# Optimization experiments

Hardware: AMD Instinct MI355X
Metric: run time of the kernel (lower is better)

Reference implementation:

```python
import jax, jax.numpy as jnp
import numpy as np
import math

E = 1024
H = 16
R = 16
ALPHA = 16
SCALING = ALPHA / R
T, B, S = 2048, 2, 2048


def setup_inputs() -> dict:
    key = jax.random.key(0)
    ks = jax.random.split(key, 20)
    d = {
        "query": jax.random.normal(ks[0], (T, B, E), jnp.float32),
        "key": jax.random.normal(ks[1], (S, B, E), jnp.float32),
        "value": jax.random.normal(ks[2], (S, B, E), jnp.float32),
    }
    i = 3
    for name in ("q", "k", "v", "o"):
        d[name + "_w"] = jax.random.normal(ks[i], (E, E), jnp.float32) * 0.02; i += 1
        d[name + "_b"] = jax.random.normal(ks[i], (E,), jnp.float32) * 0.02; i += 1
        d[name + "_la"] = jax.random.normal(ks[i], (R, E), jnp.float32) * 0.02; i += 1
        d[name + "_lb"] = jax.random.normal(ks[i], (E, R), jnp.float32) * 0.02; i += 1
    return d


def _lora_linear(x, w, b, la, lb):
    # y = x @ w.T + b + scaling * (x @ la.T) @ lb.T
    return x @ w.T + b + SCALING * ((x @ la.T) @ lb.T)


def reference(query, key, value,
              q_w, q_b, q_la, q_lb,
              k_w, k_b, k_la, k_lb,
              v_w, v_b, v_la, v_lb,
              o_w, o_b, o_la, o_lb):
    tgt_len, bsz, embed_dim = query.shape
    src_len = key.shape[0]
    head_dim = embed_dim // H
    q = _lora_linear(query, q_w, q_b, q_la, q_lb)
    k = _lora_linear(key, k_w, k_b, k_la, k_lb)
    v = _lora_linear(value, v_w, v_b, v_la, v_lb)
    # (T, B, E) -> (B*H, T, hd)
    q = q.reshape(tgt_len, bsz * H, head_dim).transpose(1, 0, 2)
    k = k.reshape(src_len, bsz * H, head_dim).transpose(1, 0, 2)
    v = v.reshape(src_len, bsz * H, head_dim).transpose(1, 0, 2)
    scale = 1.0 / math.sqrt(float(head_dim))
    scores = jnp.einsum("btd,bsd->bts", q * scale, k)  # (B*H, T, S)
    attn = jax.nn.softmax(scores, axis=-1)
    out = jnp.einsum("bts,bsd->btd", attn, v)  # (B*H, T, hd)
    out = out.transpose(1, 0, 2).reshape(tgt_len * bsz, embed_dim)
    out = _lora_linear(out, o_w, o_b, o_la, o_lb)
    out = out.reshape(tgt_len, bsz, embed_dim)
    attn_w = attn.reshape(bsz, H, tgt_len, src_len).mean(axis=1)
    return out, attn_w
```

## Files before the change

### kernel.cpp

```cpp
#include <hip/hip_runtime.h>
#include <stdint.h>

#define E_DIM 1024
#define KAUG 1056
#define N_HEADS 16
#define HD 64
#define R_LORA 16
#define T_LEN 2048
#define B_SZ 2
#define S_LEN 2048
#define NROW 4096
#define Q_SCALE 0.1803368801111204f

#define XG_N ((size_t)NROW * KAUG)
#define WG_N ((size_t)E_DIM * KAUG)
#define HSZ  ((size_t)B_SZ * N_HEADS * T_LEN * HD)

typedef unsigned short USH;
typedef __bf16 bf16x8 __attribute__((ext_vector_type(8)));
typedef unsigned short ushort8 __attribute__((ext_vector_type(8)));
typedef float  f32x4  __attribute__((ext_vector_type(4)));
typedef float  f32x16 __attribute__((ext_vector_type(16)));
typedef unsigned int u32x2 __attribute__((ext_vector_type(2)));
typedef unsigned int u32x4 __attribute__((ext_vector_type(4)));

__device__ __forceinline__ USH f2bf(float f) {
    uint32_t u = __builtin_bit_cast(uint32_t, f);
    return (USH)((u + 0x7FFFu + ((u >> 16) & 1u)) >> 16);
}
__device__ __forceinline__ float bf2f(USH s) {
    uint32_t u = ((uint32_t)s) << 16;
    return __builtin_bit_cast(float, u);
}
__device__ __forceinline__ void async_cp16(const void* g, void* l) {
    __builtin_amdgcn_global_load_lds(
        (const __attribute__((address_space(1))) void*)g,
        (__attribute__((address_space(3))) void*)l, 16, 0, 0);
}
__device__ __forceinline__ uint32_t pack_bf_trunc(float x, float y) {
    return __builtin_amdgcn_perm(__builtin_bit_cast(uint32_t, y),
                                 __builtin_bit_cast(uint32_t, x), 0x07060302u);
}
__device__ __forceinline__ bf16x8 cvt8(float4 a, float4 b) {
    ushort8 u;
    u[0] = f2bf(a.x); u[1] = f2bf(a.y); u[2] = f2bf(a.z); u[3] = f2bf(a.w);
    u[4] = f2bf(b.x); u[5] = f2bf(b.y); u[6] = f2bf(b.z); u[7] = f2bf(b.w);
    return __builtin_bit_cast(bf16x8, u);
}

__global__ __launch_bounds__(256) void lora_aug_x3_kernel(
    const float* __restrict__ Xq, const float* __restrict__ Xk,
    const float* __restrict__ Xv,
    const float* __restrict__ laq, const float* __restrict__ lak,
    const float* __restrict__ lav, USH* __restrict__ Xg_base) {
    int n0 = blockIdx.x * 16, y = blockIdx.y, tid = threadIdx.x;
    const float* X  = (y == 0) ? Xq : (y == 1) ? Xk : Xv;
    const float* la = (y == 0) ? laq : (y == 1) ? lak : lav;
    USH* Xg = Xg_base + (size_t)y * XG_N;

    int w = tid >> 6, lane = tid & 63, quad = lane >> 4, l16 = lane & 15;

    const float* xrow = X + (size_t)(n0 + l16) * E_DIM;
    const float* lrow = la + (size_t)l16 * E_DIM;
    USH* grow = Xg + (size_t)(n0 + l16) * KAUG;

    const f32x4 fzero = {0.f, 0.f, 0.f, 0.f};
    f32x4 acc = fzero;

#pragma unroll
    for (int i = 0; i < 8; ++i) {
        int k = w * 256 + i * 32 + quad * 8;
        bf16x8 af = cvt8(*(const float4*)(xrow + k), *(const float4*)(xrow + k + 4));
        *(bf16x8*)(grow + k) = af;
        bf16x8 bf_ = cvt8(*(const float4*)(lrow + k), *(const float4*)(lrow + k + 4));
        acc = __builtin_amdgcn_mfma_f32_16x16x32_bf16(af, bf_, acc, 0, 0, 0);
    }

    __shared__ float red[4][16][17];
#pragma unroll
    for (int r = 0; r < 4; ++r) red[w][quad * 4 + r][l16] = acc[r];
    __syncthreads();

    int row = tid >> 4, col = tid & 15;
    float v = red[0][row][col] + red[1][row][col] + red[2][row][col] + red[3][row][col];
    USH* trow = Xg + (size_t)(n0 + row) * KAUG + 1024;
    trow[col] = f2bf(v);
    trow[16 + col] = (col == 0) ? f2bf(1.0f) : (USH)0;
}

__global__ __launch_bounds__(256) void lora_a_bf16_kernel(
    USH* __restrict__ Xg, const float* __restrict__ la) {
    int n0 = blockIdx.x * 16, tid = threadIdx.x;
    int w = tid >> 6, lane = tid & 63, quad = lane >> 4, l16 = lane & 15;

    const USH* grow = Xg + (size_t)(n0 + l16) * KAUG;
    const float* lrow = la + (size_t)l16 * E_DIM;

    const f32x4 fzero = {0.f, 0.f, 0.f, 0.f};
    f32x4 acc = fzero;

#pragma unroll
    for (int i = 0; i < 8; ++i) {
        int k = w * 256 + i * 32 + quad * 8;
        bf16x8 af = *(const bf16x8*)(grow + k);
        bf16x8 bf_ = cvt8(*(const float4*)(lrow + k), *(const float4*)(lrow + k + 4));
        acc = __builtin_amdgcn_mfma_f32_16x16x32_bf16(af, bf_, acc, 0, 0, 0);
    }

    __shared__ float red[4][16][17];
#pragma unroll
    for (int r = 0; r < 4; ++r) red[w][quad * 4 + r][l16] = acc[r];
    __syncthreads();

    int row = tid >> 4, col = tid & 15;
    float v = red[0][row][col] + red[1][row][col] + red[2][row][col] + red[3][row][col];
    USH* trow = Xg + (size_t)(n0 + row) * KAUG + 1024;
    trow[col] = f2bf(v);
    trow[16 + col] = (col == 0) ? f2bf(1.0f) : (USH)0;
}

__global__ __launch_bounds__(256) void aug_w4_kernel(
    const float* __restrict__ Wq, const float* __restrict__ lbq, const float* __restrict__ bq,
    const float* __restrict__ Wk, const float* __restrict__ lbk, const float* __restrict__ bk_,
    const float* __restrict__ Wv, const float* __restrict__ lbv, const float* __restrict__ bv_,
    const float* __restrict__ Wo, const float* __restrict__ lbo, const float* __restrict__ bo,
    USH* __restrict__ Wg_base) {
    int e = blockIdx.x, y = blockIdx.y, tid = threadIdx.x;
    const float* W    = (y == 0) ? Wq : (y == 1) ? Wk : (y == 2) ? Wv : Wo;
    const float* lb   = (y == 0) ? lbq : (y == 1) ? lbk : (y == 2) ? lbv : lbo;
    const float* bias = (y == 0) ? bq : (y == 1) ? bk_ : (y == 2) ? bv_ : bo;
    USH* Wg = Wg_base + (size_t)y * WG_N;

    float4 v = *(const float4*)(W + (size_t)e * E_DIM + tid * 4);
    ushort4 o;
    o.x = f2bf(v.x); o.y = f2bf(v.y); o.z = f2bf(v.z); o.w = f2bf(v.w);
    *(ushort4*)(Wg + (size_t)e * KAUG + tid * 4) = o;
    if (tid < 32) {
        float t = (tid < R_LORA) ? lb[(size_t)e * R_LORA + tid]
                                 : (tid == R_LORA ? bias[e] : 0.0f);
        Wg[(size_t)e * KAUG + 1024 + tid] = f2bf(t);
    }
}

__global__ __launch_bounds__(256) void gemm_qkv_kernel(
    const USH* __restrict__ Xg_base, const USH* __restrict__ Wg_base,
    USH* __restrict__ qkv_base) {
    __shared__ __align__(16) USH As[2][128 * 32];
    __shared__ __align__(16) USH Bs[2][128 * 32];

    int orig = blockIdx.x + (blockIdx.y << 3) + blockIdx.z * 256;
    int v_ = (orig & 7) * 96 + (orig >> 3);
    int e0 = (v_ & 7) * 128, n0 = ((v_ >> 3) & 31) * 128, z = v_ >> 8;

    const USH* Xg = Xg_base + (size_t)z * XG_N;
    const USH* Wg = Wg_base + (size_t)z * WG_N;
    USH* out = qkv_base + (size_t)z * HSZ;
    float scale = (z == 0) ? Q_SCALE : 1.0f;

    int tid = threadIdx.x;
    int wid = tid >> 6, lane = tid & 63, quad = lane >> 4, l16 = lane & 15;
    int wm = wid & 1, wn = wid >> 1;

    int r0 = wid * 16 + (lane >> 2);
    int k8 = (lane & 3) * 8;

    f32x4 acc[4][4];
    const f32x4 fzero = {0.f, 0.f, 0.f, 0.f};
#pragma unroll
    for (int i = 0; i < 4; ++i)
#pragma unroll
        for (int j = 0; j < 4; ++j) acc[i][j] = fzero;

    async_cp16(Xg + (size_t)(n0 + r0) * KAUG + k8,       As[0] + (wid * 16) * 32);
    async_cp16(Xg + (size_t)(n0 + 64 + r0) * KAUG + k8,  As[0] + (64 + wid * 16) * 32);
    async_cp16(Wg + (size_t)(e0 + r0) * KAUG + k8,       Bs[0] + (wid * 16) * 32);
    async_cp16(Wg + (size_t)(e0 + 64 + r0) * KAUG + k8,  Bs[0] + (64 + wid * 16) * 32);
    __syncthreads();

    int cur = 0;
    for (int kt = 0; kt < KAUG; kt += 32, cur ^= 1) {
        if (kt + 32 < KAUG) {
            int kn = kt + 32;
            async_cp16(Xg + (size_t)(n0 + r0) * KAUG + kn + k8,       As[cur ^ 1] + (wid * 16) * 32);
            async_cp16(Xg + (size_t)(n0 + 64 + r0) * KAUG + kn + k8,  As[cur ^ 1] + (64 + wid * 16) * 32);
            async_cp16(Wg + (size_t)(e0 + r0) * KAUG + kn + k8,       Bs[cur ^ 1] + (wid * 16) * 32);
            async_cp16(Wg + (size_t)(e0 + 64 + r0) * KAUG + kn + k8,  Bs[cur ^ 1] + (64 + wid * 16) * 32);
        }

        bf16x8 af[4], bfr[4];
#pragma unroll
        for (int i = 0; i < 4; ++i)
            af[i] = *(const bf16x8*)&As[cur][(wm * 64 + i * 16 + l16) * 32 + quad * 8];
#pragma unroll
        for (int j = 0; j < 4; ++j)
            bfr[j] = *(const bf16x8*)&Bs[cur][(wn * 64 + j * 16 + l16) * 32 + quad * 8];
#pragma unroll
        for (int i = 0; i < 4; ++i)
#pragma unroll
            for (int j = 0; j < 4; ++j)
                acc[i][j] = __builtin_amdgcn_mfma_f32_16x16x32_bf16(
                    af[i], bfr[j], acc[i][j], 0, 0, 0);

        __syncthreads();
    }

#pragma unroll
    for (int i = 0; i < 4; ++i) {
#pragma unroll
        for (int j = 0; j < 4; ++j) {
#pragma unroll
            for (int r = 0; r < 4; ++r) {
                int nr = n0 + wm * 64 + i * 16 + quad * 4 + r;
                int ec = e0 + wn * 64 + j * 16 + l16;
                float v = acc[i][j][r] * scale;
                int b = nr & 1, h = ec >> 6, d = ec & 63;
                if (z != 2) {
                    int t = nr >> 1;
                    out[(((size_t)(b * 16 + h) * T_LEN + t) << 6) + d] = f2bf(v);
                } else {
                    int s = nr >> 1;
                    out[(((size_t)(b * 16 + h) * HD + d) << 11) + s] = f2bf(v);
                }
            }
        }
    }
}

__global__ __launch_bounds__(256) void gemm_o_kernel(
    const USH* __restrict__ Xg, const USH* __restrict__ Wg,
    float* __restrict__ out) {
    __shared__ __align__(16) USH As[2][64 * 32];
    __shared__ __align__(16) USH Bs[2][128 * 32];

    int orig = blockIdx.x + (blockIdx.y << 3);
    int v_ = ((orig & 7) << 6) + (orig >> 3);
    int e0 = (v_ & 7) * 128, n0 = (v_ >> 3) * 64;

    int tid = threadIdx.x;
    int wid = tid >> 6, lane = tid & 63, quad = lane >> 4, l16 = lane & 15;
    int wm = wid & 1, wn = wid >> 1;
    int r0 = wid * 16 + (lane >> 2);
    int k8 = (lane & 3) * 8;

    f32x4 acc[2][4];
    const f32x4 fzero = {0.f, 0.f, 0.f, 0.f};
#pragma unroll
    for (int i = 0; i < 2; ++i)
#pragma unroll
        for (int j = 0; j < 4; ++j) acc[i][j] = fzero;

    async_cp16(Xg + (size_t)(n0 + r0) * KAUG + k8,       As[0] + (wid * 16) * 32);
    async_cp16(Wg + (size_t)(e0 + r0) * KAUG + k8,       Bs[0] + (wid * 16) * 32);
    async_cp16(Wg + (size_t)(e0 + 64 + r0) * KAUG + k8,  Bs[0] + (64 + wid * 16) * 32);
    __syncthreads();

    int cur = 0;
    for (int kt = 0; kt < KAUG; kt += 32, cur ^= 1) {
        if (kt + 32 < KAUG) {
            int kn = kt + 32;
            async_cp16(Xg + (size_t)(n0 + r0) * KAUG + kn + k8,       As[cur ^ 1] + (wid * 16) * 32);
            async_cp16(Wg + (size_t)(e0 + r0) * KAUG + kn + k8,       Bs[cur ^ 1] + (wid * 16) * 32);
            async_cp16(Wg + (size_t)(e0 + 64 + r0) * KAUG + kn + k8,  Bs[cur ^ 1] + (64 + wid * 16) * 32);
        }

        bf16x8 af[2], bfr[4];
#pragma unroll
        for (int i = 0; i < 2; ++i)
            af[i] = *(const bf16x8*)&As[cur][(wm * 32 + i * 16 + l16) * 32 + quad * 8];
#pragma unroll
        for (int j = 0; j < 4; ++j)
            bfr[j] = *(const bf16x8*)&Bs[cur][(wn * 64 + j * 16 + l16) * 32 + quad * 8];
#pragma unroll
        for (int i = 0; i < 2; ++i)
#pragma unroll
            for (int j = 0; j < 4; ++j)
                acc[i][j] = __builtin_amdgcn_mfma_f32_16x16x32_bf16(
                    af[i], bfr[j], acc[i][j], 0, 0, 0);

        __syncthreads();
    }

#pragma unroll
    for (int i = 0; i < 2; ++i)
#pragma unroll
        for (int j = 0; j < 4; ++j)
#pragma unroll
            for (int r = 0; r < 4; ++r) {
                int nr = n0 + wm * 32 + i * 16 + quad * 4 + r;
                int ec = e0 + wn * 64 + j * 16 + l16;
                out[(size_t)nr * E_DIM + ec] = acc[i][j][r];
            }
}

__global__ __launch_bounds__(256, 2) void flash_mfma_kernel(
    const USH* __restrict__ qp, const USH* __restrict__ kp,
    const USH* __restrict__ vpt, USH* __restrict__ ohg,
    float* __restrict__ lbuf) {
    __shared__ __align__(16) USH Ks[2][4096];
    __shared__ __align__(16) USH Vs[2][4096];

    int orig = blockIdx.x + (blockIdx.y << 4);
    int v_ = ((orig & 7) << 6) + (orig >> 3);
    int t0 = (v_ & 15) * 128, bh = v_ >> 4;

    int tid = threadIdx.x, w = tid >> 6, lane = tid & 63;
    int lo = lane & 31, hi = lane >> 5;
    size_t headO = (size_t)bh * (T_LEN * HD);
    int t_base = t0 + w * 32;

    bf16x8 bq[4];
    {
        const USH* qrow = qp + headO + (size_t)(t_base + lo) * HD + hi * 8;
#pragma unroll
        for (int kb = 0; kb < 4; ++kb)
            bq[kb] = *(const bf16x8*)(qrow + kb * 16);
    }

#pragma unroll
    for (int c = 0; c < 2; ++c) {
        int f = w * 2 + c;
        async_cp16(kp + headO + (size_t)((f >> 2) * 32 + lo) * HD + (f & 3) * 16 + hi * 8,
                   &Ks[0][f * 512]);
    }
    __syncthreads();

    const f32x16 z16 = {0,0,0,0,0,0,0,0,0,0,0,0,0,0,0,0};
    f32x16 o0 = z16, o1 = z16;
    float lsum = 0.f;
    bf16x8 pa_prev[4];

    for (int it = 0; it < S_LEN / 64; ++it) {
        int cur = it & 1;
        if (it + 1 < S_LEN / 64) {
            int sn = (it + 1) * 64;
#pragma unroll
            for (int c = 0; c < 2; ++c) {
                int f = w * 2 + c;
                async_cp16(kp + headO + (size_t)(sn + (f >> 2) * 32 + lo) * HD + (f & 3) * 16 + hi * 8,
                           &Ks[cur ^ 1][f * 512]);
            }
        }
        {
            int s0 = it * 64;
#pragma unroll
            for (int c = 0; c < 2; ++c) {
                int f = w * 2 + c;
                async_cp16(vpt + headO + (size_t)((f >> 2) * 32 + lo) * S_LEN + s0 + (f & 3) * 16 + hi * 8,
                           &Vs[cur][f * 512]);
            }
        }

        f32x16 sc0 = z16, sc1 = z16;
        __builtin_amdgcn_s_setprio(1);
#pragma unroll
        for (int kb = 0; kb < 4; ++kb) {
            bf16x8 ak0 = *(const bf16x8*)&Ks[cur][(0 * 4 + kb) * 512 + lane * 8];
            sc0 = __builtin_amdgcn_mfma_f32_32x32x16_bf16(ak0, bq[kb], sc0, 0, 0, 0);
        }
#pragma unroll
        for (int kb = 0; kb < 4; ++kb) {
            bf16x8 ak1 = *(const bf16x8*)&Ks[cur][(1 * 4 + kb) * 512 + lane * 8];
            sc1 = __builtin_amdgcn_mfma_f32_32x32x16_bf16(ak1, bq[kb], sc1, 0, 0, 0);
        }

        if (it > 0) {
#pragma unroll
            for (int ks = 0; ks < 4; ++ks) {
                bf16x8 bv0 = *(const bf16x8*)&Vs[cur ^ 1][(0 * 4 + ks) * 512 + lane * 8];
                o0 = __builtin_amdgcn_mfma_f32_32x32x16_bf16(pa_prev[ks], bv0, o0, 0, 0, 0);
            }
#pragma unroll
            for (int ks = 0; ks < 4; ++ks) {
                bf16x8 bv1 = *(const bf16x8*)&Vs[cur ^ 1][(1 * 4 + ks) * 512 + lane * 8];
                o1 = __builtin_amdgcn_mfma_f32_32x32x16_bf16(pa_prev[ks], bv1, o1, 0, 0, 0);
            }
        }
        __builtin_amdgcn_s_setprio(0);

        float ls0 = 0.f, ls1 = 0.f, ls2 = 0.f, ls3 = 0.f;
#pragma unroll
        for (int r = 0; r < 16; ++r) {
            float p0 = __builtin_amdgcn_exp2f(sc0[r]);
            float p1 = __builtin_amdgcn_exp2f(sc1[r]);
            sc0[r] = p0; sc1[r] = p1;
            if ((r & 3) == 0)      { ls0 += p0; ls0 += p1; }
            else if ((r & 3) == 1) { ls1 += p0; ls1 += p1; }
            else if ((r & 3) == 2) { ls2 += p0; ls2 += p1; }
            else                   { ls3 += p0; ls3 += p1; }
        }
        lsum += (ls0 + ls1) + (ls2 + ls3);

#pragma unroll
        for (int st = 0; st < 2; ++st) {
#pragma unroll
            for (int hh = 0; hh < 2; ++hh) {
                const f32x16& s_ = st ? sc1 : sc0;
                uint32_t a0 = pack_bf_trunc(s_[hh * 8 + 0], s_[hh * 8 + 1]);
                uint32_t a1 = pack_bf_trunc(s_[hh * 8 + 2], s_[hh * 8 + 3]);
                uint32_t a2 = pack_bf_trunc(s_[hh * 8 + 4], s_[hh * 8 + 5]);
                uint32_t a3 = pack_bf_trunc(s_[hh * 8 + 6], s_[hh * 8 + 7]);
                u32x2 r02 = __builtin_amdgcn_permlane32_swap(a0, a2, false, false);
                u32x2 r13 = __builtin_amdgcn_permlane32_swap(a1, a3, false, false);
                u32x4 pd = {r02[0], r13[0], r02[1], r13[1]};
                pa_prev[st * 2 + hh] = __builtin_bit_cast(bf16x8, pd);
            }
        }

        __syncthreads();
    }

    {
#pragma unroll
        for (int ks = 0; ks < 4; ++ks) {
            bf16x8 bv0 = *(const bf16x8*)&Vs[1][(0 * 4 + ks) * 512 + lane * 8];
            o0 = __builtin_amdgcn_mfma_f32_32x32x16_bf16(pa_prev[ks], bv0, o0, 0, 0, 0);
        }
#pragma unroll
        for (int ks = 0; ks < 4; ++ks) {
            bf16x8 bv1 = *(const bf16x8*)&Vs[1][(1 * 4 + ks) * 512 + lane * 8];
            o1 = __builtin_amdgcn_mfma_f32_32x32x16_bf16(pa_prev[ks], bv1, o1, 0, 0, 0);
        }
    }

    lsum += __shfl_xor(lsum, 32, 64);
    float rinv = 1.0f / lsum;

    int b = bh >> 4, h = bh & 15;
    float inv[16];
#pragma unroll
    for (int r = 0; r < 16; ++r) {
        int rr = (r & 3) + 8 * (r >> 2) + 4 * hi;
        inv[r] = __shfl(rinv, rr, 64);
    }
#pragma unroll
    for (int r = 0; r < 16; ++r) {
        int t = t_base + (r & 3) + 8 * (r >> 2) + 4 * hi;
        size_t nrow = (size_t)(t * 2 + b) * KAUG + h * 64;
        ohg[nrow + lo]      = f2bf(o0[r] * inv[r]);
        ohg[nrow + 32 + lo] = f2bf(o1[r] * inv[r]);
    }
    if (lane < 32)
        lbuf[(size_t)bh * T_LEN + t_base + lane] = rinv;
}

__global__ __launch_bounds__(256, 4) void attnw_mfma_kernel(
    const USH* __restrict__ qp, const USH* __restrict__ kp,
    const float* __restrict__ lbuf, float* __restrict__ aw) {
    __shared__ __align__(16) USH Ks[2][4096];

    int orig = blockIdx.x + (blockIdx.y << 5) + (blockIdx.z << 9);
    int v_ = ((orig & 7) << 7) + (orig >> 3);
    int s0 = (v_ & 31) * 64, t0 = ((v_ >> 5) & 15) * 128, b = v_ >> 9;

    int tid = threadIdx.x, w = tid >> 6, lane = tid & 63;
    int quad = lane >> 4, l16 = lane & 15;

    const f32x4 fzero = {0.f, 0.f, 0.f, 0.f};
    f32x4 acc[2][4];
#pragma unroll
    for (int i2 = 0; i2 < 2; ++i2)
#pragma unroll
        for (int j = 0; j < 4; ++j) acc[i2][j] = fzero;

    {
        size_t head0 = (size_t)(b * 16) * (T_LEN * HD);
#pragma unroll
        for (int half = 0; half < 2; ++half)
            async_cp16(kp + head0 + (size_t)(s0 + w * 16 + l16) * HD + half * 32 + quad * 8,
                       &Ks[0][w * 1024 + half * 512]);
    }
    __syncthreads();

    for (int h = 0; h < N_HEADS; ++h) {
        int bh = b * 16 + h;
        size_t head = (size_t)bh * (T_LEN * HD);
        int cur = h & 1;

        if (h + 1 < N_HEADS) {
            size_t headn = head + (size_t)(T_LEN * HD);
#pragma unroll
            for (int half = 0; half < 2; ++half)
                async_cp16(kp + headn + (size_t)(s0 + w * 16 + l16) * HD + half * 32 + quad * 8,
                           &Ks[cur ^ 1][w * 1024 + half * 512]);
        }

        bf16x8 aq[2][2];
#pragma unroll
        for (int i2 = 0; i2 < 2; ++i2) {
            int i = w * 2 + i2;
            const USH* qrow = qp + head + (size_t)(t0 + i * 16 + l16) * HD + quad * 8;
            aq[i2][0] = *(const bf16x8*)qrow;
            aq[i2][1] = *(const bf16x8*)(qrow + 32);
        }

        float il[2][4];
#pragma unroll
        for (int i2 = 0; i2 < 2; ++i2)
#pragma unroll
            for (int r = 0; r < 4; ++r) {
                int t = t0 + w * 32 + i2 * 16 + quad * 4 + r;
                il[i2][r] = lbuf[(size_t)bh * T_LEN + t];
            }

        bf16x8 bk[4][2];
#pragma unroll
        for (int j = 0; j < 4; ++j)
#pragma unroll
            for (int half = 0; half < 2; ++half)
                bk[j][half] = *(const bf16x8*)&Ks[cur][j * 1024 + half * 512 + quad * 128 + l16 * 8];

#pragma unroll
        for (int i2 = 0; i2 < 2; ++i2) {
#pragma unroll
            for (int j = 0; j < 4; ++j) {
                f32x4 s = __builtin_amdgcn_mfma_f32_16x16x32_bf16(aq[i2][0], bk[j][0], fzero, 0, 0, 0);
                s = __builtin_amdgcn_mfma_f32_16x16x32_bf16(aq[i2][1], bk[j][1], s, 0, 0, 0);
#pragma unroll
                for (int r = 0; r < 4; ++r)
                    acc[i2][j][r] += __builtin_amdgcn_exp2f(s[r]) * il[i2][r];
            }
        }

        __syncthreads();
    }

    const float inv_h = 1.0f / (float)N_HEADS;
#pragma unroll
    for (int i2 = 0; i2 < 2; ++i2)
#pragma unroll
        for (int j = 0; j < 4; ++j)
#pragma unroll
            for (int r = 0; r < 4; ++r) {
                int t = t0 + w * 32 + i2 * 16 + quad * 4 + r;
                aw[(size_t)b * T_LEN * S_LEN + (size_t)t * S_LEN + s0 + j * 16 + l16] =
                    acc[i2][j][r] * inv_h;
            }
}

extern "C" void kernel_launch(void* const* d_in, const int* in_sizes, int n_in,
                              void* d_out, int out_size, void* d_ws, size_t ws_size,
                              hipStream_t stream) {
    (void)in_sizes; (void)n_in; (void)out_size; (void)ws_size;

    const float* query = (const float*)d_in[0];
    const float* key_  = (const float*)d_in[1];
    const float* value = (const float*)d_in[2];
    const float* q_w = (const float*)d_in[3],  *q_b = (const float*)d_in[4];
    const float* q_la = (const float*)d_in[5], *q_lb = (const float*)d_in[6];
    const float* k_w = (const float*)d_in[7],  *k_b = (const float*)d_in[8];
    const float* k_la = (const float*)d_in[9], *k_lb = (const float*)d_in[10];
    const float* v_w = (const float*)d_in[11], *v_b = (const float*)d_in[12];
    const float* v_la = (const float*)d_in[13], *v_lb = (const float*)d_in[14];
    const float* o_w = (const float*)d_in[15], *o_b = (const float*)d_in[16];
    const float* o_la = (const float*)d_in[17], *o_lb = (const float*)d_in[18];

    USH* Xg   = (USH*)d_ws;
    USH* Wg   = Xg + 3 * XG_N;
    USH* qkv  = Wg + 4 * WG_N;
    USH* qp   = qkv;
    USH* kp   = qkv + HSZ;
    USH* vpt  = qkv + 2 * HSZ;
    float* lbuf = (float*)(qkv + 3 * HSZ);

    float* out = (float*)d_out;
    float* aw  = out + (size_t)T_LEN * B_SZ * E_DIM;

    dim3 blk(256);

    lora_aug_x3_kernel<<<dim3(NROW / 16, 3), blk, 0, stream>>>(
        query, key_, value, q_la, k_la, v_la, Xg);
    aug_w4_kernel<<<dim3(E_DIM, 4), blk, 0, stream>>>(
        q_w, q_lb, q_b, k_w, k_lb, k_b, v_w, v_lb, v_b, o_w, o_lb, o_b, Wg);
    gemm_qkv_kernel<<<dim3(E_DIM / 128, NROW / 128, 3), blk, 0, stream>>>(Xg, Wg, qkv);

    flash_mfma_kernel<<<dim3(T_LEN / 128, B_SZ * N_HEADS), blk, 0, stream>>>(
        qp, kp, vpt, Xg, lbuf);
    attnw_mfma_kernel<<<dim3(S_LEN / 64, T_LEN / 128, B_SZ), blk, 0, stream>>>(
        qp, kp, lbuf, aw);

    lora_a_bf16_kernel<<<NROW / 16, blk, 0, stream>>>(Xg, o_la);
    gemm_o_kernel<<<dim3(E_DIM / 128, NROW / 64), blk, 0, stream>>>(
        Xg, Wg + 3 * WG_N, out);
}
```

Before: 328.7 us.

## Halve attn-weight tile rows and prefetch next head's Q and row scales

The attention-weight kernel now gives each block 64 query rows instead of 128, so each wave handles one 16-row slice and the grid doubles. The next head's Q fragments and inverse row sums are loaded into registers one iteration ahead, overlapping global latency with the current head's MFMA and exp work. MFMAs are grouped before the exp accumulation, and the launch-bounds occupancy hint is dropped. In exchange, each K tile in shared memory is reused by half as many rows, so total K traffic doubles.

```diff
diff --git a/kernel.cpp b/kernel.cpp
--- a/kernel.cpp
+++ b/kernel.cpp
@@ -443,64 +443,60 @@
         lbuf[(size_t)bh * T_LEN + t_base + lane] = rinv;
 }
 
-__global__ __launch_bounds__(256, 4) void attnw_mfma_kernel(
+__global__ __launch_bounds__(256) void attnw_mfma_kernel(
     const USH* __restrict__ qp, const USH* __restrict__ kp,
     const float* __restrict__ lbuf, float* __restrict__ aw) {
     __shared__ __align__(16) USH Ks[2][4096];
 
-    int orig = blockIdx.x + (blockIdx.y << 5) + (blockIdx.z << 9);
-    int v_ = ((orig & 7) << 7) + (orig >> 3);
-    int s0 = (v_ & 31) * 64, t0 = ((v_ >> 5) & 15) * 128, b = v_ >> 9;
+    int orig = blockIdx.x + (blockIdx.y << 5) + (blockIdx.z << 10);
+    int v_ = ((orig & 7) << 8) + (orig >> 3);
+    int s0 = (v_ & 31) * 64, t0 = ((v_ >> 5) & 31) * 64, b = v_ >> 10;
 
     int tid = threadIdx.x, w = tid >> 6, lane = tid & 63;
     int quad = lane >> 4, l16 = lane & 15;
 
     const f32x4 fzero = {0.f, 0.f, 0.f, 0.f};
-    f32x4 acc[2][4];
-#pragma unroll
-    for (int i2 = 0; i2 < 2; ++i2)
-#pragma unroll
-        for (int j = 0; j < 4; ++j) acc[i2][j] = fzero;
-
+    f32x4 acc[4];
+#pragma unroll
+    for (int j = 0; j < 4; ++j) acc[j] = fzero;
+
+    size_t head0 = (size_t)(b * 16) * (T_LEN * HD);
+
+#pragma unroll
+    for (int half = 0; half < 2; ++half)
+        async_cp16(kp + head0 + (size_t)(s0 + w * 16 + l16) * HD + half * 32 + quad * 8,
+                   &Ks[0][w * 1024 + half * 512]);
+    bf16x8 aq0, aq1;
     {
-        size_t head0 = (size_t)(b * 16) * (T_LEN * HD);
-#pragma unroll
-        for (int half = 0; half < 2; ++half)
-            async_cp16(kp + head0 + (size_t)(s0 + w * 16 + l16) * HD + half * 32 + quad * 8,
-                       &Ks[0][w * 1024 + half * 512]);
-    }
+        const USH* qrow = qp + head0 + (size_t)(t0 + w * 16 + l16) * HD + quad * 8;
+        aq0 = *(const bf16x8*)qrow;
+        aq1 = *(const bf16x8*)(qrow + 32);
+    }
+    float il[4];
+#pragma unroll
+    for (int r = 0; r < 4; ++r)
+        il[r] = lbuf[(size_t)(b * 16) * T_LEN + t0 + w * 16 + quad * 4 + r];
     __syncthreads();
 
     for (int h = 0; h < N_HEADS; ++h) {
-        int bh = b * 16 + h;
-        size_t head = (size_t)bh * (T_LEN * HD);
         int cur = h & 1;
-
+        size_t head = head0 + (size_t)h * (T_LEN * HD);
+
+        bf16x8 aq0n = aq0, aq1n = aq1;
+        float iln[4] = {il[0], il[1], il[2], il[3]};
         if (h + 1 < N_HEADS) {
             size_t headn = head + (size_t)(T_LEN * HD);
 #pragma unroll
             for (int half = 0; half < 2; ++half)
                 async_cp16(kp + headn + (size_t)(s0 + w * 16 + l16) * HD + half * 32 + quad * 8,
                            &Ks[cur ^ 1][w * 1024 + half * 512]);
-        }
-
-        bf16x8 aq[2][2];
-#pragma unroll
-        for (int i2 = 0; i2 < 2; ++i2) {
-            int i = w * 2 + i2;
-            const USH* qrow = qp + head + (size_t)(t0 + i * 16 + l16) * HD + quad * 8;
-            aq[i2][0] = *(const bf16x8*)qrow;
-            aq[i2][1] = *(const bf16x8*)(qrow + 32);
-        }
-
-        float il[2][4];
-#pragma unroll
-        for (int i2 = 0; i2 < 2; ++i2)
-#pragma unroll
-            for (int r = 0; r < 4; ++r) {
-                int t = t0 + w * 32 + i2 * 16 + quad * 4 + r;
-                il[i2][r] = lbuf[(size_t)bh * T_LEN + t];
-            }
+            const USH* qrow = qp + headn + (size_t)(t0 + w * 16 + l16) * HD + quad * 8;
+            aq0n = *(const bf16x8*)qrow;
+            aq1n = *(const bf16x8*)(qrow + 32);
+#pragma unroll
+            for (int r = 0; r < 4; ++r)
+                iln[r] = lbuf[(size_t)(b * 16 + h + 1) * T_LEN + t0 + w * 16 + quad * 4 + r];
+        }
 
         bf16x8 bk[4][2];
 #pragma unroll
@@ -509,32 +505,34 @@
             for (int half = 0; half < 2; ++half)
                 bk[j][half] = *(const bf16x8*)&Ks[cur][j * 1024 + half * 512 + quad * 128 + l16 * 8];
 
-#pragma unroll
-        for (int i2 = 0; i2 < 2; ++i2) {
-#pragma unroll
-            for (int j = 0; j < 4; ++j) {
-                f32x4 s = __builtin_amdgcn_mfma_f32_16x16x32_bf16(aq[i2][0], bk[j][0], fzero, 0, 0, 0);
-                s = __builtin_amdgcn_mfma_f32_16x16x32_bf16(aq[i2][1], bk[j][1], s, 0, 0, 0);
-#pragma unroll
-                for (int r = 0; r < 4; ++r)
-                    acc[i2][j][r] += __builtin_amdgcn_exp2f(s[r]) * il[i2][r];
-            }
-        }
+        f32x4 sc[4];
+#pragma unroll
+        for (int j = 0; j < 4; ++j) {
+            f32x4 s = __builtin_amdgcn_mfma_f32_16x16x32_bf16(aq0, bk[j][0], fzero, 0, 0, 0);
+            sc[j] = __builtin_amdgcn_mfma_f32_16x16x32_bf16(aq1, bk[j][1], s, 0, 0, 0);
+        }
+#pragma unroll
+        for (int j = 0; j < 4; ++j)
+#pragma unroll
+            for (int r = 0; r < 4; ++r)
+                acc[j][r] += __builtin_amdgcn_exp2f(sc[j][r]) * il[r];
+
+        aq0 = aq0n; aq1 = aq1n;
+#pragma unroll
+        for (int r = 0; r < 4; ++r) il[r] = iln[r];
 
         __syncthreads();
     }
 
     const float inv_h = 1.0f / (float)N_HEADS;
 #pragma unroll
-    for (int i2 = 0; i2 < 2; ++i2)
-#pragma unroll
-        for (int j = 0; j < 4; ++j)
-#pragma unroll
-            for (int r = 0; r < 4; ++r) {
-                int t = t0 + w * 32 + i2 * 16 + quad * 4 + r;
-                aw[(size_t)b * T_LEN * S_LEN + (size_t)t * S_LEN + s0 + j * 16 + l16] =
-                    acc[i2][j][r] * inv_h;
-            }
+    for (int j = 0; j < 4; ++j)
+#pragma unroll
+        for (int r = 0; r < 4; ++r) {
+            int t = t0 + w * 16 + quad * 4 + r;
+            aw[(size_t)b * T_LEN * S_LEN + (size_t)t * S_LEN + s0 + j * 16 + l16] =
+                acc[j][r] * inv_h;
+        }
 }
 
 extern "C" void kernel_launch(void* const* d_in, const int* in_sizes, int n_in,
@@ -575,7 +573,7 @@
 
     flash_mfma_kernel<<<dim3(T_LEN / 128, B_SZ * N_HEADS), blk, 0, stream>>>(
         qp, kp, vpt, Xg, lbuf);
-    attnw_mfma_kernel<<<dim3(S_LEN / 64, T_LEN / 128, B_SZ), blk, 0, stream>>>(
+    attnw_mfma_kernel<<<dim3(S_LEN / 64, T_LEN / 64, B_SZ), blk, 0, stream>>>(
         qp, kp, lbuf, aw);
 
     lora_a_bf16_kernel<<<NROW / 16, blk, 0, stream>>>(Xg, o_la);
```

After: 386.8 us. 17.7% more time.
